# Performance work log

Measured on AMD Instinct MI355X. Metric: run time of the kernel, lower is better.

The kernel has to match this reference:

```python
import jax, jax.numpy as jnp
import numpy as np

B, T, D, F, C = 16384, 256, 8, 512, 16  # batch, trees, depth, features, classes
L = 2 ** D  # leaves per tree


def setup_inputs() -> dict:
    key = jax.random.key(0)
    k1, k2, k3, k4 = jax.random.split(key, 4)
    x = jax.random.normal(k1, (B, F), dtype=jnp.float32)
    feature_weights = jax.random.normal(k2, (T, D, F), dtype=jnp.float32)
    thresholds = jax.random.normal(k3, (T, D), dtype=jnp.float32)
    responses = jax.random.normal(k4, (T, L, C), dtype=jnp.float32)
    return {"x": x, "feature_weights": feature_weights,
            "thresholds": thresholds, "responses": responses}


def reference(x, feature_weights, thresholds, responses):
    # Hard feature selection per (tree, level): argmax over features.
    fidx = jnp.argmax(feature_weights, axis=-1)            # [T, D] int
    fv = x[:, fidx]                                        # [B, T, D] gather
    bits = (fv > thresholds[None, :, :]).astype(x.dtype)   # [B, T, D]
    # decision = sum_d bit_d * 2^(D-1-d)  (matches decision*2+bit loop)
    powers = (2 ** jnp.arange(D - 1, -1, -1)).astype(x.dtype)  # [D]
    decision = jnp.sum(bits * powers, axis=-1).astype(jnp.int32)  # [B, T]
    # Gather leaf responses per (sample, tree) and average over trees.
    tree_ids = jnp.arange(T)[None, :]                      # [1, T]
    leaf_out = responses[tree_ids, decision]               # [B, T, C]
    out = jnp.mean(leaf_out, axis=1)                       # [B, C]
    return out  # dropout is identity at eval time
```

## Files before the change

### kernel.cpp

```cpp
#include <hip/hip_runtime.h>

constexpr int B = 16384;
constexpr int T = 256;
constexpr int D = 8;
constexpr int F = 512;
constexpr int C = 16;
constexpr int L = 256;

typedef float f32x4 __attribute__((ext_vector_type(4)));

struct FP { int fidx; float thr; };

__global__ __launch_bounds__(256) void node_prep_kernel(
    const float* __restrict__ fw,
    const float* __restrict__ thr,
    FP* __restrict__ packed)
{
    const int wave = threadIdx.x >> 6;
    const int lane = threadIdx.x & 63;
    const int row  = blockIdx.x * 4 + wave;
    const float* base = fw + (size_t)row * F;

    float best = -INFINITY;
    int bidx = 0;
#pragma unroll
    for (int k = 0; k < F / 64; ++k) {
        const int idx = lane + k * 64;
        const float v = base[idx];
        if (v > best) { best = v; bidx = idx; }
    }
#pragma unroll
    for (int off = 32; off >= 1; off >>= 1) {
        const float ov = __shfl_xor(best, off);
        const int   oi = __shfl_xor(bidx, off);
        if (ov > best || (ov == best && oi < bidx)) { best = ov; bidx = oi; }
    }
    if (lane == 0) {
        FP p;
        p.fidx = bidx;
        p.thr  = thr[row];
        packed[row] = p;
    }
}

__device__ __forceinline__ unsigned int bf16_rne(float f) {
    const unsigned int u = __float_as_uint(f);
    return (u + 0x7fffu + ((u >> 16) & 1u)) >> 16;
}
__global__ __launch_bounds__(256) void convert_kernel(
    const float* __restrict__ resp,
    unsigned int* __restrict__ rb)
{
    const int i = blockIdx.x * 256 + threadIdx.x;
    const float4* s = reinterpret_cast<const float4*>(resp) + i * 2;
    const float4 a = s[0], b = s[1];
    uint4 o;
    o.x = bf16_rne(a.x) | (bf16_rne(a.y) << 16);
    o.y = bf16_rne(a.z) | (bf16_rne(a.w) << 16);
    o.z = bf16_rne(b.x) | (bf16_rne(b.y) << 16);
    o.w = bf16_rne(b.z) | (bf16_rne(b.w) << 16);
    reinterpret_cast<uint4*>(rb)[i] = o;
}

__global__ __launch_bounds__(256) void decide_kernel(
    const float* __restrict__ x,
    const FP* __restrict__ packed,
    unsigned int* __restrict__ dec)
{
    __shared__ float xrow[4][F];
    __shared__ unsigned char sdec[4][T];

    const int b0  = blockIdx.x * 4;
    const int tid = threadIdx.x;

    {
        const float4* xs = reinterpret_cast<const float4*>(x + (size_t)b0 * F);
        float4* xl = reinterpret_cast<float4*>(&xrow[0][0]);
        xl[tid]       = xs[tid];
        xl[tid + 256] = xs[tid + 256];
    }
    __syncthreads();

    {
        const int2* p2 = reinterpret_cast<const int2*>(packed) + tid * D;
        int2 raw[D];
#pragma unroll
        for (int d = 0; d < D; ++d) raw[d] = p2[d];
        int dec0 = 0, dec1 = 0, dec2 = 0, dec3 = 0;
#pragma unroll
        for (int d = 0; d < D; ++d) {
            const int   f  = raw[d].x;
            const float th = __int_as_float(raw[d].y);
            const int   p  = 128 >> d;
            dec0 |= (xrow[0][f] > th) ? p : 0;
            dec1 |= (xrow[1][f] > th) ? p : 0;
            dec2 |= (xrow[2][f] > th) ? p : 0;
            dec3 |= (xrow[3][f] > th) ? p : 0;
        }
        sdec[0][tid] = (unsigned char)dec0;
        sdec[1][tid] = (unsigned char)dec1;
        sdec[2][tid] = (unsigned char)dec2;
        sdec[3][tid] = (unsigned char)dec3;
    }
    __syncthreads();

    dec[blockIdx.x * 256 + tid] = reinterpret_cast<const unsigned int*>(&sdec[0][0])[tid];
}

__global__ __launch_bounds__(256, 4) void gather_kernel(
    const unsigned int* __restrict__ dec,
    const unsigned short* __restrict__ rb,
    float* __restrict__ out)
{
    const int tid  = threadIdx.x;
    const int w    = tid >> 6;
    const int lane = tid & 63;
    const int s    = blockIdx.x * 4 + w;

    const unsigned int w0 = dec[s * 64 + lane];

    const int wsel = lane >> 4;
    const int bsel = ((lane >> 2) & 3) * 8;
    const int lbase = ((lane >> 2) << 12) | ((lane & 3) << 2);

    int dw[16];
#pragma unroll
    for (int kk = 0; kk < 16; ++kk) dw[kk] = __shfl((int)w0, 4 * kk + wsel);

    uint2 r[16];
#pragma unroll
    for (int kk = 0; kk < 16; ++kk) {
        const int dd = (dw[kk] >> bsel) & 255;
        r[kk] = *reinterpret_cast<const uint2*>(rb + (kk << 16) + (dd << 4) + lbase);
    }

    float4 acc = make_float4(0.f, 0.f, 0.f, 0.f);
#pragma unroll
    for (int kk = 0; kk < 16; ++kk) {
        acc.x += __uint_as_float(r[kk].x << 16);
        acc.y += __uint_as_float(r[kk].x & 0xffff0000u);
        acc.z += __uint_as_float(r[kk].y << 16);
        acc.w += __uint_as_float(r[kk].y & 0xffff0000u);
    }

#pragma unroll
    for (int off = 4; off <= 32; off <<= 1) {
        acc.x += __shfl_xor(acc.x, off);
        acc.y += __shfl_xor(acc.y, off);
        acc.z += __shfl_xor(acc.z, off);
        acc.w += __shfl_xor(acc.w, off);
    }

    if (lane < 4) {
        const float sc = 1.0f / T;
        f32x4 o = { acc.x * sc, acc.y * sc, acc.z * sc, acc.w * sc };
        *reinterpret_cast<f32x4*>(out + ((size_t)s << 4) + (lane << 2)) = o;
    }
}

extern "C" void kernel_launch(void* const* d_in, const int* in_sizes, int n_in,
                              void* d_out, int out_size, void* d_ws, size_t ws_size,
                              hipStream_t stream) {
    const float* x         = (const float*)d_in[0];
    const float* fw        = (const float*)d_in[1];
    const float* thr       = (const float*)d_in[2];
    const float* responses = (const float*)d_in[3];
    float* out             = (float*)d_out;

    FP* packed          = (FP*)d_ws;
    unsigned int* dec   = (unsigned int*)((char*)d_ws + (1 << 16));
    unsigned int* rb    = (unsigned int*)((char*)d_ws + (5 << 20));

    node_prep_kernel<<<(T * D) / 4, 256, 0, stream>>>(fw, thr, packed);
    convert_kernel<<<(T * L * C) / 8 / 256, 256, 0, stream>>>(responses, rb);
    decide_kernel<<<B / 4, 256, 0, stream>>>(x, packed, dec);
    gather_kernel<<<B / 4, 256, 0, stream>>>(dec, (const unsigned short*)rb, out);
}
```

Before: 109.2 us.

## Fuse prep kernels and merge decision with leaf gather via shared memory

```diff
diff --git a/kernel.cpp b/kernel.cpp
--- a/kernel.cpp
+++ b/kernel.cpp
@@ -11,61 +11,62 @@
 
 struct FP { int fidx; float thr; };
 
-__global__ __launch_bounds__(256) void node_prep_kernel(
-    const float* __restrict__ fw,
-    const float* __restrict__ thr,
-    FP* __restrict__ packed)
-{
-    const int wave = threadIdx.x >> 6;
-    const int lane = threadIdx.x & 63;
-    const int row  = blockIdx.x * 4 + wave;
-    const float* base = fw + (size_t)row * F;
-
-    float best = -INFINITY;
-    int bidx = 0;
-#pragma unroll
-    for (int k = 0; k < F / 64; ++k) {
-        const int idx = lane + k * 64;
-        const float v = base[idx];
-        if (v > best) { best = v; bidx = idx; }
-    }
-#pragma unroll
-    for (int off = 32; off >= 1; off >>= 1) {
-        const float ov = __shfl_xor(best, off);
-        const int   oi = __shfl_xor(bidx, off);
-        if (ov > best || (ov == best && oi < bidx)) { best = ov; bidx = oi; }
-    }
-    if (lane == 0) {
-        FP p;
-        p.fidx = bidx;
-        p.thr  = thr[row];
-        packed[row] = p;
-    }
-}
-
 __device__ __forceinline__ unsigned int bf16_rne(float f) {
     const unsigned int u = __float_as_uint(f);
     return (u + 0x7fffu + ((u >> 16) & 1u)) >> 16;
 }
-__global__ __launch_bounds__(256) void convert_kernel(
+
+__global__ __launch_bounds__(256) void prep_kernel(
+    const float* __restrict__ fw,
+    const float* __restrict__ thr,
     const float* __restrict__ resp,
+    FP* __restrict__ packed,
     unsigned int* __restrict__ rb)
 {
-    const int i = blockIdx.x * 256 + threadIdx.x;
-    const float4* s = reinterpret_cast<const float4*>(resp) + i * 2;
-    const float4 a = s[0], b = s[1];
-    uint4 o;
-    o.x = bf16_rne(a.x) | (bf16_rne(a.y) << 16);
-    o.y = bf16_rne(a.z) | (bf16_rne(a.w) << 16);
-    o.z = bf16_rne(b.x) | (bf16_rne(b.y) << 16);
-    o.w = bf16_rne(b.z) | (bf16_rne(b.w) << 16);
-    reinterpret_cast<uint4*>(rb)[i] = o;
+    if (blockIdx.x < 512) {
+        const int wave = threadIdx.x >> 6;
+        const int lane = threadIdx.x & 63;
+        const int row  = blockIdx.x * 4 + wave;
+        const float* base = fw + (size_t)row * F;
+
+        float best = -INFINITY;
+        int bidx = 0;
+#pragma unroll
+        for (int k = 0; k < F / 64; ++k) {
+            const int idx = lane + k * 64;
+            const float v = base[idx];
+            if (v > best) { best = v; bidx = idx; }
+        }
+#pragma unroll
+        for (int off = 32; off >= 1; off >>= 1) {
+            const float ov = __shfl_xor(best, off);
+            const int   oi = __shfl_xor(bidx, off);
+            if (ov > best || (ov == best && oi < bidx)) { best = ov; bidx = oi; }
+        }
+        if (lane == 0) {
+            FP p;
+            p.fidx = bidx;
+            p.thr  = thr[row];
+            packed[row] = p;
+        }
+    } else {
+        const int i = (blockIdx.x - 512) * 256 + threadIdx.x;
+        const float4* s = reinterpret_cast<const float4*>(resp) + i * 2;
+        const float4 a = s[0], b = s[1];
+        uint4 o;
+        o.x = bf16_rne(a.x) | (bf16_rne(a.y) << 16);
+        o.y = bf16_rne(a.z) | (bf16_rne(a.w) << 16);
+        o.z = bf16_rne(b.x) | (bf16_rne(b.y) << 16);
+        o.w = bf16_rne(b.z) | (bf16_rne(b.w) << 16);
+        reinterpret_cast<uint4*>(rb)[i] = o;
+    }
 }
 
-__global__ __launch_bounds__(256) void decide_kernel(
+__global__ __launch_bounds__(256, 4) void forest_kernel(
     const float* __restrict__ x,
     const FP* __restrict__ packed,
-    unsigned int* __restrict__ dec)
+    const unsigned short* __restrict__ rb,
+    float* __restrict__ out)
 {
     __shared__ float xrow[4][F];
     __shared__ unsigned char sdec[4][T];
@@ -104,28 +105,17 @@
     }
     __syncthreads();
 
-    dec[blockIdx.x * 256 + tid] = reinterpret_cast<const unsigned int*>(&sdec[0][0])[tid];
-}
-
-__global__ __launch_bounds__(256, 4) void gather_kernel(
-    const unsigned int* __restrict__ dec,
-    const unsigned short* __restrict__ rb,
-    float* __restrict__ out)
-{
-    const int tid  = threadIdx.x;
     const int w    = tid >> 6;
     const int lane = tid & 63;
-    const int s    = blockIdx.x * 4 + w;
 
-    const unsigned int w0 = dec[s * 64 + lane];
-
+    const int* pw  = reinterpret_cast<const int*>(&sdec[w][0]);
     const int wsel = lane >> 4;
     const int bsel = ((lane >> 2) & 3) * 8;
     const int lbase = ((lane >> 2) << 12) | ((lane & 3) << 2);
 
     int dw[16];
 #pragma unroll
-    for (int kk = 0; kk < 16; ++kk) dw[kk] = __shfl((int)w0, 4 * kk + wsel);
+    for (int kk = 0; kk < 16; ++kk) dw[kk] = pw[4 * kk + wsel];
 
     uint2 r[16];
 #pragma unroll
@@ -154,7 +144,7 @@
     if (lane < 4) {
         const float sc = 1.0f / T;
         f32x4 o = { acc.x * sc, acc.y * sc, acc.z * sc, acc.w * sc };
-        *reinterpret_cast<f32x4*>(out + ((size_t)s << 4) + (lane << 2)) = o;
+        *reinterpret_cast<f32x4*>(out + ((size_t)(b0 + w) << 4) + (lane << 2)) = o;
     }
 }
 
@@ -167,12 +157,10 @@
     const float* responses = (const float*)d_in[3];
     float* out             = (float*)d_out;
 
-    FP* packed          = (FP*)d_ws;
-    unsigned int* dec   = (unsigned int*)((char*)d_ws + (1 << 16));
-    unsigned int* rb    = (unsigned int*)((char*)d_ws + (5 << 20));
+    FP* packed        = (FP*)d_ws;
+    unsigned int* rb  = (unsigned int*)((char*)d_ws + (1 << 16));
 
-    node_prep_kernel<<<(T * D) / 4, 256, 0, stream>>>(fw, thr, packed);
-    convert_kernel<<<(T * L * C) / 8 / 256, 256, 0, stream>>>(responses, rb);
-    decide_kernel<<<B / 4, 256, 0, stream>>>(x, packed, dec);
-    gather_kernel<<<B / 4, 256, 0, stream>>>(dec, (const unsigned short*)rb, out);
+    prep_kernel<<<1024, 256, 0, stream>>>(fw, thr, responses, packed, rb);
+    forest_kernel<<<B / 4, 256, 0, stream>>>(x, packed,
+                                             (const unsigned short*)rb, out);
 }
```

Result: faster. 101.7 us (-6.9%).
